# Optimization experiments

Measured on AMD Instinct MI355X. Metric: run time of the kernel, lower is better.

## Reference

```python
import jax, jax.numpy as jnp
import numpy as np

B, T, C = 4, 1024, 1024
H, HKV, D = 16, 4, 64
GATE_CH = 12
ROPE_THETA = 10000.0


def _rms_norm(x):
    # F.rms_norm with default eps = machine epsilon of dtype, no learnable scale
    eps = jnp.finfo(x.dtype).eps
    ms = jnp.mean(jnp.square(x), axis=-1, keepdims=True)
    return x * jax.lax.rsqrt(ms + eps)


def _apply_rotary(x, cos, sin):
    # x: (B, T, h, D); cos/sin: (1, T, 1, D//2). Half-split rotation.
    d = x.shape[-1] // 2
    x1, x2 = x[..., :d], x[..., d:]
    y1 = x1 * cos + x2 * sin
    y2 = -x1 * sin + x2 * cos
    return jnp.concatenate([y1, y2], axis=-1)


def setup_inputs() -> dict:
    key = jax.random.key(0)
    ks = jax.random.split(key, 8)
    x = jax.random.normal(ks[0], (B, T, C), dtype=jnp.float32)
    ve = jax.random.normal(ks[1], (B, T, HKV * D), dtype=jnp.float32)
    # real RoPE tables, shape (1, T, 1, D//2)
    half = D // 2
    inv_freq = 1.0 / (ROPE_THETA ** (np.arange(half, dtype=np.float32) / half))
    freqs = np.arange(T, dtype=np.float32)[:, None] * inv_freq[None, :]
    cos = jnp.asarray(np.cos(freqs), dtype=jnp.float32).reshape(1, T, 1, half)
    sin = jnp.asarray(np.sin(freqs), dtype=jnp.float32).reshape(1, T, 1, half)
    s = 0.02
    Wq = jax.random.normal(ks[2], (H * D, C), dtype=jnp.float32) * s
    Wk = jax.random.normal(ks[3], (HKV * D, C), dtype=jnp.float32) * s
    Wv = jax.random.normal(ks[4], (HKV * D, C), dtype=jnp.float32) * s
    Wo = jax.random.normal(ks[5], (C, C), dtype=jnp.float32) * s
    Wg = jax.random.normal(ks[6], (HKV, GATE_CH), dtype=jnp.float32) * s
    return {"x": x, "ve": ve, "cos": cos, "sin": sin,
            "Wq": Wq, "Wk": Wk, "Wv": Wv, "Wo": Wo, "Wg": Wg,
            "window_size": 256}


def reference(x, ve, cos, sin, Wq, Wk, Wv, Wo, Wg, window_size):
    b, t, c = x.shape
    d = 2 * cos.shape[-1]
    h = Wq.shape[0] // d
    hkv = Wk.shape[0] // d
    rep = h // hkv

    q = (x @ Wq.T).reshape(b, t, h, d)
    k = (x @ Wk.T).reshape(b, t, hkv, d)
    v = (x @ Wv.T).reshape(b, t, hkv, d)

    # value-embedding sigmoid gate (3 * sigmoid of first 12 channels of x)
    gate = 3.0 * jax.nn.sigmoid(x[..., : Wg.shape[1]] @ Wg.T)  # (b, t, hkv)
    v = v + gate[..., None] * ve.reshape(b, t, hkv, d)

    q = _apply_rotary(q, cos, sin)
    k = _apply_rotary(k, cos, sin)
    q = _rms_norm(q) * 1.2
    k = _rms_norm(k) * 1.2

    # GQA attention with sliding-window causal mask (left=window_size, right=0)
    qg = q.reshape(b, t, hkv, rep, d)
    scale = 1.0 / jnp.sqrt(jnp.asarray(d, dtype=q.dtype))
    scores = jnp.einsum('bqgrd,bkgd->bgrqk', qg, k) * scale
    i = jnp.arange(t)[:, None]
    j = jnp.arange(t)[None, :]
    mask = (j <= i) & ((i - j) <= window_size)  # (t, t)
    scores = jnp.where(mask[None, None, None], scores, -jnp.inf)
    probs = jax.nn.softmax(scores, axis=-1)
    y = jnp.einsum('bgrqk,bkgd->bqgrd', probs, v).reshape(b, t, h * d)
    return y @ Wo.T
```

## Files before the change

kernel.cpp:

```cpp
#include <hip/hip_runtime.h>

typedef __bf16 v8bf __attribute__((ext_vector_type(8)));
typedef float v4f __attribute__((ext_vector_type(4)));
typedef unsigned int v4u __attribute__((ext_vector_type(4)));
typedef unsigned int v2u __attribute__((ext_vector_type(2)));
typedef unsigned short u16;

#define DEVI static __device__ __forceinline__

DEVI float bf2f(u16 u) {
    union { float f; unsigned int i; } c; c.i = ((unsigned int)u) << 16; return c.f;
}
DEVI u16 f2bf(float f) {
    union { __bf16 b; u16 u; } c; c.b = (__bf16)f;
    return c.u;
}

union Frag { v4u u; v8bf v; u16 h[8]; };

#define GLD16(gptr, lptr) __builtin_amdgcn_global_load_lds( \
    (const __attribute__((address_space(1))) void*)(gptr),  \
    (__attribute__((address_space(3))) void*)(lptr), 16, 0, 0)

__global__ __launch_bounds__(256) void convert6(
    const float* __restrict__ x, const float* __restrict__ wq,
    const float* __restrict__ wk, const float* __restrict__ wv,
    const float* __restrict__ wo, const float* __restrict__ Wg,
    u16* __restrict__ xb, u16* __restrict__ wb, u16* __restrict__ wob,
    float* __restrict__ gates)
{
    if (blockIdx.y == 5) {
        const int stride = gridDim.x * 256;
        for (int i = blockIdx.x * 256 + threadIdx.x; i < 4096 * 4; i += stride) {
            const int token = i >> 2, g = i & 3;
            float dot = 0.f;
#pragma unroll
            for (int c = 0; c < 12; c++)
                dot += x[token * 1024 + c] * Wg[g * 12 + c];
            gates[i] = 3.f / (1.f + __expf(-dot));
        }
        return;
    }
    const float* src; u16* dst; int n;
    switch (blockIdx.y) {
        case 0: src = x;  dst = xb;               n = 4096 * 1024; break;
        case 1: src = wq; dst = wb;               n = 1024 * 1024; break;
        case 2: src = wk; dst = wb + 1024 * 1024; n = 256 * 1024;  break;
        case 3: src = wv; dst = wb + 1280 * 1024; n = 256 * 1024;  break;
        default: src = wo; dst = wob;             n = 1024 * 1024; break;
    }
    const int stride = gridDim.x * 256 * 4;
    for (int i = (blockIdx.x * 256 + threadIdx.x) * 4; i < n; i += stride) {
        const float4 f = *(const float4*)(src + i);
        v2u p;
        p[0] = (unsigned int)f2bf(f.x) | ((unsigned int)f2bf(f.y) << 16);
        p[1] = (unsigned int)f2bf(f.z) | ((unsigned int)f2bf(f.w) << 16);
        *(v2u*)(dst + i) = p;
    }
}

template <bool QKV>
__global__ __launch_bounds__(256) void gemm_bt(
    const u16* __restrict__ A, const u16* __restrict__ B,
    void* __restrict__ Cv, int N,
    const float* __restrict__ cs, const float* __restrict__ sn,
    const float* __restrict__ gates, const float* __restrict__ ve,
    u16* __restrict__ qn, u16* __restrict__ kn, u16* __restrict__ vn)
{
    __shared__ __align__(16) u16 As[64 * 64];
    __shared__ __align__(16) u16 Bs[128 * 64];
    const int tid  = threadIdx.x;
    const int lane = tid & 63, l15 = lane & 15, quad = (lane >> 4) & 3;
    const int w    = tid >> 6;
    const int wr   = (w >> 1) * 32, wc = (w & 1) * 64;
    const int m0   = blockIdx.x * 64, n0 = blockIdx.y * 128;

    const u16* ab = A + m0 * 1024;
    const u16* bb = B + n0 * 1024;
    const int r0 = tid >> 3;
    const int c0 = (tid & 7) * 8;
    const u16* ag = ab + r0 * 1024 + c0;
    const u16* bg = bb + r0 * 1024 + c0;
    u16* al = &As[r0 * 64 + c0];
    u16* bl = &Bs[r0 * 64 + c0];

    v4f acc[2][4];
    const v4f vzero = {0.f, 0.f, 0.f, 0.f};
#pragma unroll
    for (int i = 0; i < 2; i++)
#pragma unroll
        for (int j = 0; j < 4; j++) acc[i][j] = vzero;

    for (int k0 = 0; k0 < 1024; k0 += 64) {
        __syncthreads();
        GLD16(ag + k0,             al);
        GLD16(ag + k0 + 32 * 1024, al + 32 * 64);
        GLD16(bg + k0,             bl);
        GLD16(bg + k0 + 32 * 1024, bl + 32 * 64);
        GLD16(bg + k0 + 64 * 1024, bl + 64 * 64);
        GLD16(bg + k0 + 96 * 1024, bl + 96 * 64);
        __syncthreads();
#pragma unroll
        for (int ks = 0; ks < 2; ks++) {
            v8bf af[2];
#pragma unroll
            for (int mi = 0; mi < 2; mi++)
                af[mi] = *(const v8bf*)&As[(wr + mi * 16 + l15) * 64 + ks * 32 + quad * 8];
#pragma unroll
            for (int ni = 0; ni < 4; ni++) {
                v8bf bv = *(const v8bf*)&Bs[(wc + ni * 16 + l15) * 64 + ks * 32 + quad * 8];
#pragma unroll
                for (int mi = 0; mi < 2; mi++)
                    acc[mi][ni] = __builtin_amdgcn_mfma_f32_16x16x32_bf16(af[mi], bv, acc[mi][ni], 0, 0, 0);
            }
        }
    }

    if (!QKV) {
#pragma unroll
        for (int mi = 0; mi < 2; mi++) {
            const int row = m0 + wr + mi * 16 + quad * 4;
#pragma unroll
            for (int ni = 0; ni < 4; ni++) {
                const int col = n0 + wc + ni * 16 + l15;
#pragma unroll
                for (int r = 0; r < 4; r++)
                    ((float*)Cv)[(row + r) * N + col] = acc[mi][ni][r];
            }
        }
        return;
    }

    const int hcol = n0 + wc;
    if (hcol < 1280) {
        const bool isQ = (hcol < 1024);
        u16* dst = isQ ? (qn + (hcol >> 6) * 64) : (kn + ((hcol - 1024) >> 6) * 64);
        const int dstride = isQ ? 1024 : 256;
#pragma unroll
        for (int mi = 0; mi < 2; mi++) {
#pragma unroll
            for (int r = 0; r < 4; r++) {
                const int row = m0 + wr + mi * 16 + quad * 4 + r;
                const int pos = row & 1023;
                const float c0 = cs[pos * 32 + l15],      s0 = sn[pos * 32 + l15];
                const float c1 = cs[pos * 32 + 16 + l15], s1 = sn[pos * 32 + 16 + l15];
                const float y0 = acc[mi][0][r] * c0 + acc[mi][2][r] * s0;
                const float y2 = acc[mi][2][r] * c0 - acc[mi][0][r] * s0;
                const float y1 = acc[mi][1][r] * c1 + acc[mi][3][r] * s1;
                const float y3 = acc[mi][3][r] * c1 - acc[mi][1][r] * s1;
                float ss = y0 * y0 + y1 * y1 + y2 * y2 + y3 * y3;
#pragma unroll
                for (int off = 8; off >= 1; off >>= 1)
                    ss += __shfl_xor(ss, off, 64);
                const float inv = rsqrtf(ss * (1.0f / 64.0f) + 1.1920929e-7f) * 1.2f;
                u16* d = dst + row * dstride;
                d[l15]      = f2bf(y0 * inv);
                d[16 + l15] = f2bf(y1 * inv);
                d[32 + l15] = f2bf(y2 * inv);
                d[48 + l15] = f2bf(y3 * inv);
            }
        }
    } else {
        const int g = (hcol - 1280) >> 6;
#pragma unroll
        for (int mi = 0; mi < 2; mi++) {
#pragma unroll
            for (int r = 0; r < 4; r++) {
                const int row = m0 + wr + mi * 16 + quad * 4 + r;
                const float gate = gates[row * 4 + g];
                u16* d = vn + row * 256 + g * 64;
                const float* vesrc = ve + row * 256 + g * 64;
#pragma unroll
                for (int ni = 0; ni < 4; ni++)
                    d[ni * 16 + l15] = f2bf(acc[mi][ni][r] + gate * vesrc[ni * 16 + l15]);
            }
        }
    }
}

__global__ __launch_bounds__(256) void vtrans(
    const u16* __restrict__ vn, u16* __restrict__ vt)
{
    __shared__ __align__(16) u16 T[64 * 72];
    const int tid = threadIdx.x;
    const int t0  = blockIdx.x * 64, g = blockIdx.y, b = blockIdx.z;
    {
        const int row = tid >> 2, ch = (tid & 3) * 16;
        const int goff = (b * 1024 + t0 + row) * 256 + g * 64 + ch;
        *(v4u*)&T[row * 72 + ch]     = *(const v4u*)&vn[goff];
        *(v4u*)&T[row * 72 + ch + 8] = *(const v4u*)&vn[goff + 8];
    }
    __syncthreads();
    {
        const int d = tid >> 2, tc = (tid & 3) * 16;
        Frag o0, o1;
#pragma unroll
        for (int j = 0; j < 8; j++) {
            o0.h[j] = T[(tc + j) * 72 + d];
            o1.h[j] = T[(tc + 8 + j) * 72 + d];
        }
        u16* dst = vt + ((b * 4 + g) * 64 + d) * 1024 + t0 + tc;
        *(v4u*)dst       = o0.u;
        *(v4u*)(dst + 8) = o1.u;
    }
}

__global__ __launch_bounds__(256) void attn(
    const u16* __restrict__ qn, const u16* __restrict__ kn,
    const u16* __restrict__ vt, u16* __restrict__ yo)
{
    __shared__ __align__(16) u16 Ks[64 * 72];
    __shared__ __align__(16) u16 VTs[64 * 72];
    __shared__ __align__(16) u16 Ps[4][32 * 72];
    const int tid  = threadIdx.x;
    const int w    = tid >> 6, lane = tid & 63, l15 = lane & 15, quad = (lane >> 4) & 3;
    const int qb   = blockIdx.x, h = blockIdx.y, b = blockIdx.z;
    const int g    = h >> 2;
    const int qbase = qb * 128;
    const int qabs0 = qbase + w * 32;
    const int tok0  = b * 1024 + qabs0;
    u16* pw = Ps[w];

    v8bf qf[2][2];
#pragma unroll
    for (int mi = 0; mi < 2; mi++)
#pragma unroll
        for (int ks = 0; ks < 2; ks++) {
            Frag f;
            f.u = *(const v4u*)&qn[(tok0 + mi * 16 + l15) * 1024 + h * 64 + ks * 32 + quad * 8];
#pragma unroll
            for (int j = 0; j < 8; j++) f.h[j] = f2bf(0.18033688f * bf2f(f.h[j]));
            qf[mi][ks] = f.v;
        }

    v4f o[2][4];
    float li[2][4];
    const v4f vzero = {0.f, 0.f, 0.f, 0.f};
#pragma unroll
    for (int mi = 0; mi < 2; mi++) {
#pragma unroll
        for (int nd = 0; nd < 4; nd++) o[mi][nd] = vzero;
#pragma unroll
        for (int r = 0; r < 4; r++) li[mi][r] = 0.f;
    }

    const int kstart = (qbase >= 256) ? qbase - 256 : 0;
    const int kend   = qbase + 64;
    for (int kbase = kstart; kbase <= kend; kbase += 64) {
        __syncthreads();
        {
            const int row = tid >> 2, ch = (tid & 3) * 16;
            const int goff = (b * 1024 + kbase + row) * 256 + g * 64 + ch;
            *(v4u*)&Ks[row * 72 + ch]     = *(const v4u*)&kn[goff];
            *(v4u*)&Ks[row * 72 + ch + 8] = *(const v4u*)&kn[goff + 8];
            const u16* vsrc = vt + ((b * 4 + g) * 64 + row) * 1024 + kbase + ch;
            *(v4u*)&VTs[row * 72 + ch]     = *(const v4u*)vsrc;
            *(v4u*)&VTs[row * 72 + ch + 8] = *(const v4u*)(vsrc + 8);
        }
        __syncthreads();

        bool skip2[2][4], full2[2][4];
#pragma unroll
        for (int mi = 0; mi < 2; mi++)
#pragma unroll
            for (int ni = 0; ni < 4; ni++) {
                const int qw = qabs0 + mi * 16;
                const int left = kbase + ni * 16;
                skip2[mi][ni] = (left > qw + 15) || (qw - (left + 15) > 256);
                full2[mi][ni] = ((left + 15) <= qw) && ((qw + 15 - left) <= 256);
            }

#pragma unroll
        for (int mi = 0; mi < 2; mi++) {
#pragma unroll
            for (int ni = 0; ni < 4; ni++) {
                if (skip2[mi][ni]) {
#pragma unroll
                    for (int r = 0; r < 4; r++)
                        pw[(mi * 16 + quad * 4 + r) * 72 + ni * 16 + l15] = 0;
                    continue;
                }
                v8bf kf0 = *(const v8bf*)&Ks[(ni * 16 + l15) * 72 + quad * 8];
                v8bf kf1 = *(const v8bf*)&Ks[(ni * 16 + l15) * 72 + 32 + quad * 8];
                v4f a = vzero;
                a = __builtin_amdgcn_mfma_f32_16x16x32_bf16(qf[mi][0], kf0, a, 0, 0, 0);
                a = __builtin_amdgcn_mfma_f32_16x16x32_bf16(qf[mi][1], kf1, a, 0, 0, 0);
                if (!full2[mi][ni]) {
                    const int kj = kbase + ni * 16 + l15;
#pragma unroll
                    for (int r = 0; r < 4; r++) {
                        const int qi = qabs0 + mi * 16 + quad * 4 + r;
                        if (!((kj <= qi) && (qi - kj <= 256))) a[r] = -1e30f;
                    }
                }
#pragma unroll
                for (int r = 0; r < 4; r++) {
                    const float p = exp2f(a[r] - 17.312340f);
                    li[mi][r] += p;
                    pw[(mi * 16 + quad * 4 + r) * 72 + ni * 16 + l15] = f2bf(p);
                }
            }
        }

#pragma unroll
        for (int mi = 0; mi < 2; mi++)
#pragma unroll
            for (int ks = 0; ks < 2; ks++) {
                if (skip2[mi][2 * ks] && skip2[mi][2 * ks + 1]) continue;
                v8bf af = *(const v8bf*)&pw[(mi * 16 + l15) * 72 + ks * 32 + quad * 8];
#pragma unroll
                for (int nd = 0; nd < 4; nd++) {
                    v8bf bv = *(const v8bf*)&VTs[(nd * 16 + l15) * 72 + ks * 32 + quad * 8];
                    o[mi][nd] = __builtin_amdgcn_mfma_f32_16x16x32_bf16(af, bv, o[mi][nd], 0, 0, 0);
                }
            }
    }

#pragma unroll
    for (int mi = 0; mi < 2; mi++) {
#pragma unroll
        for (int off = 8; off >= 1; off >>= 1)
#pragma unroll
            for (int r = 0; r < 4; r++)
                li[mi][r] += __shfl_xor(li[mi][r], off, 64);
        float inv[4];
#pragma unroll
        for (int r = 0; r < 4; r++) inv[r] = 1.f / li[mi][r];
#pragma unroll
        for (int nd = 0; nd < 4; nd++) {
            const int col = h * 64 + nd * 16 + l15;
#pragma unroll
            for (int r = 0; r < 4; r++) {
                const int row = tok0 + mi * 16 + quad * 4 + r;
                yo[row * 1024 + col] = f2bf(o[mi][nd][r] * inv[r]);
            }
        }
    }
}

extern "C" void kernel_launch(void* const* d_in, const int* in_sizes, int n_in,
                              void* d_out, int out_size, void* d_ws, size_t ws_size,
                              hipStream_t stream)
{
    const float* x  = (const float*)d_in[0];
    const float* ve = (const float*)d_in[1];
    const float* cs = (const float*)d_in[2];
    const float* sn = (const float*)d_in[3];
    const float* Wq = (const float*)d_in[4];
    const float* Wk = (const float*)d_in[5];
    const float* Wv = (const float*)d_in[6];
    const float* Wo = (const float*)d_in[7];
    const float* Wg = (const float*)d_in[8];

    u16*   xb    = (u16*)d_ws;
    u16*   wb    = xb  + 4096 * 1024;
    u16*   wob   = wb  + 1536 * 1024;
    u16*   qn    = wob + 1024 * 1024;
    u16*   kn    = qn  + 4096 * 1024;
    u16*   vn    = kn  + 4096 * 256;
    u16*   vt    = vn  + 4096 * 256;
    u16*   ay    = vt  + 4096 * 256;
    float* gates = (float*)(ay + 4096 * 1024);

    convert6<<<dim3(512, 6), 256, 0, stream>>>(x, Wq, Wk, Wv, Wo, Wg, xb, wb, wob, gates);
    gemm_bt<true><<<dim3(64, 12), 256, 0, stream>>>(xb, wb, nullptr, 1536,
                                                    cs, sn, gates, ve, qn, kn, vn);
    vtrans<<<dim3(16, 4, 4), 256, 0, stream>>>(vn, vt);
    attn<<<dim3(8, 16, 4), 256, 0, stream>>>(qn, kn, vt, ay);
    gemm_bt<false><<<dim3(64, 8), 256, 0, stream>>>(ay, wob, d_out, 1024,
                                                    nullptr, nullptr, nullptr, nullptr,
                                                    nullptr, nullptr, nullptr);
}
```

Baseline: 162.7 us.

## Enlarge QKV GEMM tile to 128x128 and fuse V transpose into epilogue

The QKV projection GEMM now uses 128x128 block tiles (4x4 MFMA fragments per wave), halving the grid to 384 blocks and improving operand reuse from LDS. The V epilogue writes gated values straight into the transposed vt layout with packed 4-token stores, which removes the separate vtrans kernel and the vn intermediate buffer. The output projection is split into its own non-templated kernel with the old 64x128 tile. The larger accumulator raises register pressure, and 384 blocks may underfill the GPU's CUs.

```diff
diff --git a/kernel.cpp b/kernel.cpp
--- a/kernel.cpp
+++ b/kernel.cpp
@@ -59,21 +59,19 @@
     }
 }
 
-template <bool QKV>
-__global__ __launch_bounds__(256) void gemm_bt(
+__global__ __launch_bounds__(256) void gemm_qkv(
     const u16* __restrict__ A, const u16* __restrict__ B,
-    void* __restrict__ Cv, int N,
     const float* __restrict__ cs, const float* __restrict__ sn,
     const float* __restrict__ gates, const float* __restrict__ ve,
-    u16* __restrict__ qn, u16* __restrict__ kn, u16* __restrict__ vn)
-{
-    __shared__ __align__(16) u16 As[64 * 64];
+    u16* __restrict__ qn, u16* __restrict__ kn, u16* __restrict__ vt)
+{
+    __shared__ __align__(16) u16 As[128 * 64];
     __shared__ __align__(16) u16 Bs[128 * 64];
     const int tid  = threadIdx.x;
     const int lane = tid & 63, l15 = lane & 15, quad = (lane >> 4) & 3;
     const int w    = tid >> 6;
-    const int wr   = (w >> 1) * 32, wc = (w & 1) * 64;
-    const int m0   = blockIdx.x * 64, n0 = blockIdx.y * 128;
+    const int wr   = (w >> 1) * 64, wc = (w & 1) * 64;
+    const int m0   = blockIdx.x * 128, n0 = blockIdx.y * 128;
 
     const u16* ab = A + m0 * 1024;
     const u16* bb = B + n0 * 1024;
@@ -84,10 +82,10 @@
     u16* al = &As[r0 * 64 + c0];
     u16* bl = &Bs[r0 * 64 + c0];
 
-    v4f acc[2][4];
+    v4f acc[4][4];
     const v4f vzero = {0.f, 0.f, 0.f, 0.f};
 #pragma unroll
-    for (int i = 0; i < 2; i++)
+    for (int i = 0; i < 4; i++)
 #pragma unroll
         for (int j = 0; j < 4; j++) acc[i][j] = vzero;
 
@@ -95,6 +93,8 @@
         __syncthreads();
         GLD16(ag + k0,             al);
         GLD16(ag + k0 + 32 * 1024, al + 32 * 64);
+        GLD16(ag + k0 + 64 * 1024, al + 64 * 64);
+        GLD16(ag + k0 + 96 * 1024, al + 96 * 64);
         GLD16(bg + k0,             bl);
         GLD16(bg + k0 + 32 * 1024, bl + 32 * 64);
         GLD16(bg + k0 + 64 * 1024, bl + 64 * 64);
@@ -102,33 +102,19 @@
         __syncthreads();
 #pragma unroll
         for (int ks = 0; ks < 2; ks++) {
-            v8bf af[2];
-#pragma unroll
-            for (int mi = 0; mi < 2; mi++)
+            v8bf af[4], bv[4];
+#pragma unroll
+            for (int mi = 0; mi < 4; mi++)
                 af[mi] = *(const v8bf*)&As[(wr + mi * 16 + l15) * 64 + ks * 32 + quad * 8];
 #pragma unroll
-            for (int ni = 0; ni < 4; ni++) {
-                v8bf bv = *(const v8bf*)&Bs[(wc + ni * 16 + l15) * 64 + ks * 32 + quad * 8];
-#pragma unroll
-                for (int mi = 0; mi < 2; mi++)
-                    acc[mi][ni] = __builtin_amdgcn_mfma_f32_16x16x32_bf16(af[mi], bv, acc[mi][ni], 0, 0, 0);
-            }
-        }
-    }
-
-    if (!QKV) {
-#pragma unroll
-        for (int mi = 0; mi < 2; mi++) {
-            const int row = m0 + wr + mi * 16 + quad * 4;
-#pragma unroll
-            for (int ni = 0; ni < 4; ni++) {
-                const int col = n0 + wc + ni * 16 + l15;
-#pragma unroll
-                for (int r = 0; r < 4; r++)
-                    ((float*)Cv)[(row + r) * N + col] = acc[mi][ni][r];
-            }
-        }
-        return;
+            for (int ni = 0; ni < 4; ni++)
+                bv[ni] = *(const v8bf*)&Bs[(wc + ni * 16 + l15) * 64 + ks * 32 + quad * 8];
+#pragma unroll
+            for (int ni = 0; ni < 4; ni++)
+#pragma unroll
+                for (int mi = 0; mi < 4; mi++)
+                    acc[mi][ni] = __builtin_amdgcn_mfma_f32_16x16x32_bf16(af[mi], bv[ni], acc[mi][ni], 0, 0, 0);
+        }
     }
 
     const int hcol = n0 + wc;
@@ -137,17 +123,17 @@
         u16* dst = isQ ? (qn + (hcol >> 6) * 64) : (kn + ((hcol - 1024) >> 6) * 64);
         const int dstride = isQ ? 1024 : 256;
 #pragma unroll
-        for (int mi = 0; mi < 2; mi++) {
+        for (int mi = 0; mi < 4; mi++) {
 #pragma unroll
             for (int r = 0; r < 4; r++) {
                 const int row = m0 + wr + mi * 16 + quad * 4 + r;
                 const int pos = row & 1023;
-                const float c0 = cs[pos * 32 + l15],      s0 = sn[pos * 32 + l15];
-                const float c1 = cs[pos * 32 + 16 + l15], s1 = sn[pos * 32 + 16 + l15];
-                const float y0 = acc[mi][0][r] * c0 + acc[mi][2][r] * s0;
-                const float y2 = acc[mi][2][r] * c0 - acc[mi][0][r] * s0;
-                const float y1 = acc[mi][1][r] * c1 + acc[mi][3][r] * s1;
-                const float y3 = acc[mi][3][r] * c1 - acc[mi][1][r] * s1;
+                const float c0_ = cs[pos * 32 + l15],      s0_ = sn[pos * 32 + l15];
+                const float c1_ = cs[pos * 32 + 16 + l15], s1_ = sn[pos * 32 + 16 + l15];
+                const float y0 = acc[mi][0][r] * c0_ + acc[mi][2][r] * s0_;
+                const float y2 = acc[mi][2][r] * c0_ - acc[mi][0][r] * s0_;
+                const float y1 = acc[mi][1][r] * c1_ + acc[mi][3][r] * s1_;
+                const float y3 = acc[mi][3][r] * c1_ - acc[mi][1][r] * s1_;
                 float ss = y0 * y0 + y1 * y1 + y2 * y2 + y3 * y3;
 #pragma unroll
                 for (int off = 8; off >= 1; off >>= 1)
@@ -163,45 +149,88 @@
     } else {
         const int g = (hcol - 1280) >> 6;
 #pragma unroll
-        for (int mi = 0; mi < 2; mi++) {
-#pragma unroll
-            for (int r = 0; r < 4; r++) {
-                const int row = m0 + wr + mi * 16 + quad * 4 + r;
-                const float gate = gates[row * 4 + g];
-                u16* d = vn + row * 256 + g * 64;
-                const float* vesrc = ve + row * 256 + g * 64;
-#pragma unroll
-                for (int ni = 0; ni < 4; ni++)
-                    d[ni * 16 + l15] = f2bf(acc[mi][ni][r] + gate * vesrc[ni * 16 + l15]);
-            }
-        }
-    }
-}
-
-__global__ __launch_bounds__(256) void vtrans(
-    const u16* __restrict__ vn, u16* __restrict__ vt)
-{
-    __shared__ __align__(16) u16 T[64 * 72];
-    const int tid = threadIdx.x;
-    const int t0  = blockIdx.x * 64, g = blockIdx.y, b = blockIdx.z;
-    {
-        const int row = tid >> 2, ch = (tid & 3) * 16;
-        const int goff = (b * 1024 + t0 + row) * 256 + g * 64 + ch;
-        *(v4u*)&T[row * 72 + ch]     = *(const v4u*)&vn[goff];
-        *(v4u*)&T[row * 72 + ch + 8] = *(const v4u*)&vn[goff + 8];
-    }
-    __syncthreads();
-    {
-        const int d = tid >> 2, tc = (tid & 3) * 16;
-        Frag o0, o1;
-#pragma unroll
-        for (int j = 0; j < 8; j++) {
-            o0.h[j] = T[(tc + j) * 72 + d];
-            o1.h[j] = T[(tc + 8 + j) * 72 + d];
-        }
-        u16* dst = vt + ((b * 4 + g) * 64 + d) * 1024 + t0 + tc;
-        *(v4u*)dst       = o0.u;
-        *(v4u*)(dst + 8) = o1.u;
+        for (int mi = 0; mi < 4; mi++) {
+            const int row0 = m0 + wr + mi * 16 + quad * 4;
+            const int b_ = row0 >> 10, t_ = row0 & 1023;
+            float gate[4];
+#pragma unroll
+            for (int r = 0; r < 4; r++) gate[r] = gates[(row0 + r) * 4 + g];
+#pragma unroll
+            for (int ni = 0; ni < 4; ni++) {
+                const int d = ni * 16 + l15;
+                union { u16 h[4]; v2u u; } pk;
+#pragma unroll
+                for (int r = 0; r < 4; r++)
+                    pk.h[r] = f2bf(acc[mi][ni][r] + gate[r] * ve[(row0 + r) * 256 + g * 64 + d]);
+                *(v2u*)&vt[((b_ * 4 + g) * 64 + d) * 1024 + t_] = pk.u;
+            }
+        }
+    }
+}
+
+__global__ __launch_bounds__(256) void gemm_out(
+    const u16* __restrict__ A, const u16* __restrict__ B,
+    float* __restrict__ C, int N)
+{
+    __shared__ __align__(16) u16 As[64 * 64];
+    __shared__ __align__(16) u16 Bs[128 * 64];
+    const int tid  = threadIdx.x;
+    const int lane = tid & 63, l15 = lane & 15, quad = (lane >> 4) & 3;
+    const int w    = tid >> 6;
+    const int wr   = (w >> 1) * 32, wc = (w & 1) * 64;
+    const int m0   = blockIdx.x * 64, n0 = blockIdx.y * 128;
+
+    const u16* ab = A + m0 * 1024;
+    const u16* bb = B + n0 * 1024;
+    const int r0 = tid >> 3;
+    const int c0 = (tid & 7) * 8;
+    const u16* ag = ab + r0 * 1024 + c0;
+    const u16* bg = bb + r0 * 1024 + c0;
+    u16* al = &As[r0 * 64 + c0];
+    u16* bl = &Bs[r0 * 64 + c0];
+
+    v4f acc[2][4];
+    const v4f vzero = {0.f, 0.f, 0.f, 0.f};
+#pragma unroll
+    for (int i = 0; i < 2; i++)
+#pragma unroll
+        for (int j = 0; j < 4; j++) acc[i][j] = vzero;
+
+    for (int k0 = 0; k0 < 1024; k0 += 64) {
+        __syncthreads();
+        GLD16(ag + k0,             al);
+        GLD16(ag + k0 + 32 * 1024, al + 32 * 64);
+        GLD16(bg + k0,             bl);
+        GLD16(bg + k0 + 32 * 1024, bl + 32 * 64);
+        GLD16(bg + k0 + 64 * 1024, bl + 64 * 64);
+        GLD16(bg + k0 + 96 * 1024, bl + 96 * 64);
+        __syncthreads();
+#pragma unroll
+        for (int ks = 0; ks < 2; ks++) {
+            v8bf af[2];
+#pragma unroll
+            for (int mi = 0; mi < 2; mi++)
+                af[mi] = *(const v8bf*)&As[(wr + mi * 16 + l15) * 64 + ks * 32 + quad * 8];
+#pragma unroll
+            for (int ni = 0; ni < 4; ni++) {
+                v8bf bv = *(const v8bf*)&Bs[(wc + ni * 16 + l15) * 64 + ks * 32 + quad * 8];
+#pragma unroll
+                for (int mi = 0; mi < 2; mi++)
+                    acc[mi][ni] = __builtin_amdgcn_mfma_f32_16x16x32_bf16(af[mi], bv, acc[mi][ni], 0, 0, 0);
+            }
+        }
+    }
+
+#pragma unroll
+    for (int mi = 0; mi < 2; mi++) {
+        const int row = m0 + wr + mi * 16 + quad * 4;
+#pragma unroll
+        for (int ni = 0; ni < 4; ni++) {
+            const int col = n0 + wc + ni * 16 + l15;
+#pragma unroll
+            for (int r = 0; r < 4; r++)
+                C[(row + r) * N + col] = acc[mi][ni][r];
+        }
     }
 }
 
@@ -357,17 +386,12 @@
     u16*   wob   = wb  + 1536 * 1024;
     u16*   qn    = wob + 1024 * 1024;
     u16*   kn    = qn  + 4096 * 1024;
-    u16*   vn    = kn  + 4096 * 256;
-    u16*   vt    = vn  + 4096 * 256;
+    u16*   vt    = kn  + 4096 * 256;
     u16*   ay    = vt  + 4096 * 256;
     float* gates = (float*)(ay + 4096 * 1024);
 
     convert6<<<dim3(512, 6), 256, 0, stream>>>(x, Wq, Wk, Wv, Wo, Wg, xb, wb, wob, gates);
-    gemm_bt<true><<<dim3(64, 12), 256, 0, stream>>>(xb, wb, nullptr, 1536,
-                                                    cs, sn, gates, ve, qn, kn, vn);
-    vtrans<<<dim3(16, 4, 4), 256, 0, stream>>>(vn, vt);
+    gemm_qkv<<<dim3(32, 12), 256, 0, stream>>>(xb, wb, cs, sn, gates, ve, qn, kn, vt);
     attn<<<dim3(8, 16, 4), 256, 0, stream>>>(qn, kn, vt, ay);
-    gemm_bt<false><<<dim3(64, 8), 256, 0, stream>>>(ay, wob, d_out, 1024,
-                                                    nullptr, nullptr, nullptr, nullptr,
-                                                    nullptr, nullptr, nullptr);
-}
+    gemm_out<<<dim3(64, 8), 256, 0, stream>>>(ay, wob, (float*)d_out, 1024);
+}
```

New measurement: 164.5 us. Within noise of the previous version (+1.1%).
